# Kernel optimization log

Hardware: AMD Instinct MI355X
Metric: run time of the kernel (lower is better)

Reference implementation:

```python
import jax, jax.numpy as jnp
import numpy as np

DIM = 512
BATCH, SEQ = 4, 4096


def setup_inputs() -> dict:
    key = jax.random.key(0)
    kx, kq, kk, kv, ko = jax.random.split(key, 5)
    s = DIM ** -0.5  # fan-in style init scale for stability
    return {
        "x": jax.random.normal(kx, (BATCH, SEQ, DIM), dtype=jnp.float32),
        "Wq": jax.random.normal(kq, (DIM, DIM), dtype=jnp.float32) * s,
        "Wk": jax.random.normal(kk, (DIM, DIM), dtype=jnp.float32) * s,
        "Wv": jax.random.normal(kv, (DIM, DIM), dtype=jnp.float32) * s,
        "Wo": jax.random.normal(ko, (DIM, DIM), dtype=jnp.float32) * s,
    }


def reference(x, Wq, Wk, Wv, Wo):
    # x: [B, S, D]; projections (torch Linear, no bias -> x @ W here)
    q = jnp.einsum('bsd,dk->bsk', x, Wq)  # [B,S,K]
    k = jnp.einsum('bsd,dk->bsk', x, Wk)  # [B,S,K]
    v = jnp.einsum('bsd,dv->bsv', x, Wv)  # [B,S,V]

    # sequential recurrence: M_t = M_{t-1} + v_t k_t^T ; y_t = M_t q_t
    def step(M, qkv_t):
        q_t, k_t, v_t = qkv_t  # each [B, K] / [B, V]
        M = M + v_t[:, :, None] * k_t[:, None, :]  # [B, V, K]
        y_t = jnp.einsum('bvk,bk->bv', M, q_t)
        return M, y_t

    M0 = jnp.zeros((x.shape[0], Wv.shape[1], Wk.shape[1]), dtype=x.dtype)
    qT = jnp.swapaxes(q, 0, 1)  # [S,B,K]
    kT = jnp.swapaxes(k, 0, 1)
    vT = jnp.swapaxes(v, 0, 1)
    _, ys = jax.lax.scan(step, M0, (qT, kT, vT))  # ys: [S,B,V]
    y = jnp.swapaxes(ys, 0, 1)  # [B,S,V]
    return jnp.einsum('bsv,vd->bsd', y, Wo)
```

## Files before the change

### kernel.cpp

```cpp
#include <hip/hip_runtime.h>
#include <hip/hip_bf16.h>

typedef __attribute__((ext_vector_type(8))) short bf16x8;
typedef __attribute__((ext_vector_type(4))) float f32x4;

__device__ inline short f2bf(float f) {
    __hip_bfloat16 h = __float2bfloat16(f);
    short s;
    __builtin_memcpy(&s, &h, 2);
    return s;
}
__device__ inline float bf2f(short s) {
    unsigned int u = ((unsigned int)(unsigned short)s) << 16;
    float f;
    __builtin_memcpy(&f, &u, 4);
    return f;
}

__device__ inline void cp16_async(const void* g, void* l) {
    __builtin_amdgcn_global_load_lds(
        (const __attribute__((address_space(1))) void*)g,
        (__attribute__((address_space(3))) void*)l, 16, 0, 0);
}


__global__ void prep_kernel(const float* __restrict__ x, short* __restrict__ Xb,
                            const float* __restrict__ W0, const float* __restrict__ W1,
                            const float* __restrict__ W2, const float* __restrict__ W3,
                            short* __restrict__ W4T) {
    int bid = blockIdx.x;
    if (bid < 8192) {
        int i = bid * 256 + threadIdx.x;
        float4 f = ((const float4*)x)[i];
        union { short s[4]; int2 v; } u;
        u.s[0] = f2bf(f.x); u.s[1] = f2bf(f.y); u.s[2] = f2bf(f.z); u.s[3] = f2bf(f.w);
        ((int2*)Xb)[i] = u.v;
    } else {
        int i = (bid - 8192) * 256 + threadIdx.x;
        int w = i >> 18;
        int r = i & 262143;
        int n = r >> 9, k = r & 511;
        const float* W = (w == 0) ? W0 : (w == 1) ? W1 : (w == 2) ? W2 : W3;
        W4T[i] = f2bf(W[k * 512 + n]);
    }
}


#define LDS_DECL __shared__ short sA0[4096], sA1[4096], sB0[4096], sB1[4096]

__device__ inline void mfma_kloop64(const short* __restrict__ A, int lda,
                                    const short* __restrict__ B, int ldb,
                                    int Kd, f32x4* acc,
                                    short* sA0, short* sA1, short* sB0, short* sB1) {
    const int tid = threadIdx.x, lane = tid & 63, wv = tid >> 6;
    const int quad = lane >> 4, lr = lane & 15;
    const int wr = (wv >> 1) * 64, wc = (wv & 1) * 64;
    const int c0 = tid, c1 = tid + 256;
    const int r0 = c0 >> 2, k80 = (c0 & 3) * 8;
    const int r1 = c1 >> 2, k81 = (c1 & 3) * 8;

    for (int k0 = 0; k0 < Kd; k0 += 64) {
        __syncthreads();
        cp16_async(A + (size_t)r0 * lda + k0 + k80,      sA0 + c0 * 8);
        cp16_async(A + (size_t)r1 * lda + k0 + k81,      sA0 + c1 * 8);
        cp16_async(A + (size_t)r0 * lda + k0 + 32 + k80, sA1 + c0 * 8);
        cp16_async(A + (size_t)r1 * lda + k0 + 32 + k81, sA1 + c1 * 8);
        cp16_async(B + (size_t)r0 * ldb + k0 + k80,      sB0 + c0 * 8);
        cp16_async(B + (size_t)r1 * ldb + k0 + k81,      sB0 + c1 * 8);
        cp16_async(B + (size_t)r0 * ldb + k0 + 32 + k80, sB1 + c0 * 8);
        cp16_async(B + (size_t)r1 * ldb + k0 + 32 + k81, sB1 + c1 * 8);
        __syncthreads();
#pragma unroll
        for (int half = 0; half < 2; ++half) {
            const short* pa = half ? sA1 : sA0;
            const short* pb = half ? sB1 : sB0;
            bf16x8 af[4], bfr[4];
#pragma unroll
            for (int i = 0; i < 4; ++i)
                af[i] = *(const bf16x8*)&pa[(wr + i * 16 + lr) * 32 + quad * 8];
#pragma unroll
            for (int j = 0; j < 4; ++j)
                bfr[j] = *(const bf16x8*)&pb[(wc + j * 16 + lr) * 32 + quad * 8];
#pragma unroll
            for (int i = 0; i < 4; ++i)
#pragma unroll
                for (int j = 0; j < 4; ++j)
                    acc[i * 4 + j] = __builtin_amdgcn_mfma_f32_16x16x32_bf16(af[i], bfr[j], acc[i * 4 + j], 0, 0, 0);
        }
    }
}

__device__ inline void store_out(float* p, float v) { *p = v; }
__device__ inline void store_out(short* p, float v) { *p = f2bf(v); }

template <typename OutT>
__device__ inline void store_tile128(OutT* C, int ldc, const f32x4* acc) {
    const int lane = threadIdx.x & 63, wv = threadIdx.x >> 6;
    const int quad = lane >> 4, lr = lane & 15;
    const int wr = (wv >> 1) * 64, wc = (wv & 1) * 64;
#pragma unroll
    for (int i = 0; i < 4; ++i)
#pragma unroll
        for (int j = 0; j < 4; ++j)
#pragma unroll
            for (int r = 0; r < 4; ++r)
                store_out(&C[(size_t)(wr + i * 16 + quad * 4 + r) * ldc + wc + j * 16 + lr],
                          acc[i * 4 + j][r]);
}

__global__ __launch_bounds__(256, 4) void proj_all(const short* __restrict__ Xb,
                                                   const short* __restrict__ W4T,
                                                   short* __restrict__ Qb, short* __restrict__ Kb,
                                                   short* __restrict__ Vt, short* __restrict__ Kt) {
    LDS_DECL;
    f32x4 acc[16];
#pragma unroll
    for (int i = 0; i < 16; ++i) acc[i] = (f32x4){0.f, 0.f, 0.f, 0.f};
    const int bid = blockIdx.x;
    const int lane = threadIdx.x & 63, wv = threadIdx.x >> 6;
    const int quad = lane >> 4, lr = lane & 15;
    const int wr = (wv >> 1) * 64, wc = (wv & 1) * 64;
    if (bid < 1024) {
        const int mt = bid >> 3, by = bid & 7;
        const short* At = Xb + (size_t)mt * 128 * 512;
        const short* Bt = W4T + (size_t)by * 128 * 512;
        short* Ct = ((by < 4) ? Qb : Kb) + (size_t)mt * 128 * 512 + (by & 3) * 128;
        mfma_kloop64(At, 512, Bt, 512, 512, acc, sA0, sA1, sB0, sB1);
        store_tile128(Ct, 512, acc);
        if (by >= 4) {
            const int b = mt >> 5;
            const int t0b = (mt & 31) * 128;
            const int f0 = (by - 4) * 128;
#pragma unroll
            for (int i = 0; i < 4; ++i)
#pragma unroll
                for (int j = 0; j < 4; ++j) {
                    int f = f0 + wc + j * 16 + lr;
                    int tt0 = t0b + wr + i * 16 + quad * 4;
                    short tmp[4];
#pragma unroll
                    for (int r = 0; r < 4; ++r) tmp[r] = f2bf(acc[i * 4 + j][r]);
                    *(int2*)&Kt[((size_t)b * 512 + f) * 4096 + tt0] = *(const int2*)tmp;
                }
        }
    } else {
        const int r = bid - 1024;
        const int b = r & 3, tt = (r >> 2) & 31, ft = r >> 7;
        const short* At = W4T + (size_t)2 * 262144 + (size_t)ft * 128 * 512;
        const short* Bt = Xb + ((size_t)b * 4096 + tt * 128) * 512;
        short* Ct = Vt + (size_t)b * 512 * 4096 + (size_t)ft * 128 * 4096 + tt * 128;
        mfma_kloop64(At, 512, Bt, 512, 512, acc, sA0, sA1, sB0, sB1);
        store_tile128(Ct, 4096, acc);
    }
}


__global__ __launch_bounds__(256, 4) void phaseA(const short* __restrict__ Vt,
                                                 const short* __restrict__ Kt,
                                                 short* __restrict__ AM) {
    LDS_DECL;
    const int bc = blockIdx.z, b = bc >> 4, c = bc & 15;
    const short* Ap = Vt + ((size_t)b * 512 + blockIdx.x * 128) * 4096 + c * 256;
    const short* Bp = Kt + ((size_t)b * 512 + blockIdx.y * 128) * 4096 + c * 256;
    short* Cp = AM + (size_t)bc * 262144 + (size_t)blockIdx.x * 128 * 512 + blockIdx.y * 128;
    f32x4 acc[16];
#pragma unroll
    for (int i = 0; i < 16; ++i) acc[i] = (f32x4){0.f, 0.f, 0.f, 0.f};
    mfma_kloop64(Ap, 4096, Bp, 4096, 256, acc, sA0, sA1, sB0, sB1);
    store_tile128(Cp, 512, acc);
}

__global__ __launch_bounds__(256, 4) void scan_phaseS(short* __restrict__ AM,
                                                      const short* __restrict__ Q,
                                                      const short* __restrict__ K,
                                                      short* __restrict__ P) {
    LDS_DECL;
    if (blockIdx.x < 512) {
        int i = blockIdx.x * 256 + threadIdx.x;
        int b = i >> 15;
        int vk8 = i & 32767;
        size_t base = (size_t)b * 16 * 262144 + (size_t)vk8 * 8;
        float acc[8];
#pragma unroll
        for (int s = 0; s < 8; ++s) acc[s] = 0.f;
        for (int c = 0; c < 16; ++c) {
            short* p = AM + base + (size_t)c * 262144;
            short in8[8];
            *(int4*)in8 = *(const int4*)p;
            short out8[8];
#pragma unroll
            for (int s = 0; s < 8; ++s) out8[s] = f2bf(acc[s]);
            *(int4*)p = *(const int4*)out8;
#pragma unroll
            for (int s = 0; s < 8; ++s) acc[s] += bf2f(in8[s]);
        }
        return;
    }
    const int e = blockIdx.x - 512;
    const int bc = e >> 2, mt = e & 1, nt = (e >> 1) & 1;
    if (mt < nt) return;
    const int b = bc >> 4, c = bc & 15;
    short* Pt = P + (size_t)bc * 65536 + (size_t)mt * 128 * 256 + nt * 128;
    const short* Ap = Q + ((size_t)(b * 4096 + c * 256 + mt * 128)) * 512;
    const short* Bp = K + ((size_t)(b * 4096 + c * 256 + nt * 128)) * 512;
    f32x4 acc[16];
#pragma unroll
    for (int i = 0; i < 16; ++i) acc[i] = (f32x4){0.f, 0.f, 0.f, 0.f};
    mfma_kloop64(Ap, 512, Bp, 512, 512, acc, sA0, sA1, sB0, sB1);
    const int lane = threadIdx.x & 63, wv = threadIdx.x >> 6;
    const int quad = lane >> 4, lr = lane & 15;
    const int wr = (wv >> 1) * 64, wc = (wv & 1) * 64;
    const bool diag = (mt == nt);
#pragma unroll
    for (int i = 0; i < 4; ++i)
#pragma unroll
        for (int j = 0; j < 4; ++j)
#pragma unroll
            for (int r = 0; r < 4; ++r) {
                int t = wr + i * 16 + quad * 4 + r;
                int jj = wc + j * 16 + lr;
                float v = (!diag || jj <= t) ? acc[i * 4 + j][r] : 0.f;
                Pt[(size_t)t * 256 + jj] = f2bf(v);
            }
}

__global__ __launch_bounds__(256, 4) void phaseY(const short* __restrict__ Q,
                                                 const short* __restrict__ Mpre,
                                                 const short* __restrict__ P,
                                                 const short* __restrict__ Vt,
                                                 short* __restrict__ Y) {
    LDS_DECL;
    const int bc = blockIdx.z, b = bc >> 4, c = bc & 15;
    const int mt = blockIdx.x, nt = blockIdx.y;
    f32x4 acc[16];
#pragma unroll
    for (int i = 0; i < 16; ++i) acc[i] = (f32x4){0.f, 0.f, 0.f, 0.f};
    const short* Ai = Q + ((size_t)(b * 4096 + c * 256 + mt * 128)) * 512;
    const short* Bi = Mpre + (size_t)bc * 262144 + (size_t)nt * 128 * 512;
    mfma_kloop64(Ai, 512, Bi, 512, 512, acc, sA0, sA1, sB0, sB1);
    const short* Ap = P + (size_t)bc * 65536 + (size_t)mt * 128 * 256;
    const short* Bv = Vt + ((size_t)b * 512 + nt * 128) * 4096 + c * 256;
    mfma_kloop64(Ap, 256, Bv, 4096, (mt + 1) * 128, acc, sA0, sA1, sB0, sB1);
    short* Cp = Y + ((size_t)(b * 4096 + c * 256 + mt * 128)) * 512 + nt * 128;
    store_tile128(Cp, 512, acc);
}

template <typename OutT>
__global__ __launch_bounds__(256, 4) void gemm128(const short* __restrict__ A, int lda,
                                                  const short* __restrict__ B, int ldb,
                                                  OutT* __restrict__ C, int ldc, int Kd) {
    LDS_DECL;
    const short* At = A + (size_t)blockIdx.x * 128 * lda;
    const short* Bt = B + (size_t)blockIdx.y * 128 * ldb;
    OutT* Ct = C + (size_t)blockIdx.x * 128 * ldc + blockIdx.y * 128;
    f32x4 acc[16];
#pragma unroll
    for (int i = 0; i < 16; ++i) acc[i] = (f32x4){0.f, 0.f, 0.f, 0.f};
    mfma_kloop64(At, lda, Bt, ldb, Kd, acc, sA0, sA1, sB0, sB1);
    store_tile128(Ct, ldc, acc);
}


extern "C" void kernel_launch(void* const* d_in, const int* in_sizes, int n_in,
                              void* d_out, int out_size, void* d_ws, size_t ws_size,
                              hipStream_t stream) {
    const float* x  = (const float*)d_in[0];
    const float* Wq = (const float*)d_in[1];
    const float* Wk = (const float*)d_in[2];
    const float* Wv = (const float*)d_in[3];
    const float* Wo = (const float*)d_in[4];
    float* out = (float*)d_out;

    const size_t NTD = 16384 * 512;

    short* ws  = (short*)d_ws;
    short* Xb  = ws;
    short* Qb  = Xb + NTD;
    short* Kb  = Qb + NTD;
    short* Kt  = Kb + NTD;
    short* Vt  = Kt + NTD;
    short* P   = Vt + NTD;
    short* W4T = P + 4194304;
    short* AM  = W4T + 1048576;
    short* Yb  = Kb;

    short* WoT = W4T + 3 * 262144;

    prep_kernel<<<12288, 256, 0, stream>>>(x, Xb, Wq, Wk, Wv, Wo, W4T);
    proj_all<<<1536, 256, 0, stream>>>(Xb, W4T, Qb, Kb, Vt, Kt);
    phaseA<<<dim3(4, 4, 64), 256, 0, stream>>>(Vt, Kt, AM);
    scan_phaseS<<<768, 256, 0, stream>>>(AM, Qb, Kb, P);
    phaseY<<<dim3(2, 4, 64), 256, 0, stream>>>(Qb, AM, P, Vt, Yb);
    gemm128<float><<<dim3(128, 4), 256, 0, stream>>>(Yb, 512, WoT, 512, out, 512, 512);
}
```

Baseline: 222.0 us.

## Fuse all phases into one cooperative persistent kernel with grid syncs

Replaces the six separate kernel launches with one cooperative kernel that loops over virtual block indices for each phase, separated by grid-wide syncs. This removes per-launch overhead and the gaps between kernels. In exchange the grid is capped at 512 persistent blocks, launch bounds drop to 2 blocks per CU, and grid.sync barriers add their own cost. Phase bodies that do uneven work may also load-balance worse. The multi-kernel path is kept as a fallback if the cooperative launch fails.

```diff
diff --git a/kernel.cpp b/kernel.cpp
--- a/kernel.cpp
+++ b/kernel.cpp
@@ -1,5 +1,8 @@
 #include <hip/hip_runtime.h>
 #include <hip/hip_bf16.h>
+#include <hip/hip_cooperative_groups.h>
+
+namespace cg = cooperative_groups;
 
 typedef __attribute__((ext_vector_type(8))) short bf16x8;
 typedef __attribute__((ext_vector_type(4))) float f32x4;
@@ -23,30 +26,6 @@
         (__attribute__((address_space(3))) void*)l, 16, 0, 0);
 }
 
-
-__global__ void prep_kernel(const float* __restrict__ x, short* __restrict__ Xb,
-                            const float* __restrict__ W0, const float* __restrict__ W1,
-                            const float* __restrict__ W2, const float* __restrict__ W3,
-                            short* __restrict__ W4T) {
-    int bid = blockIdx.x;
-    if (bid < 8192) {
-        int i = bid * 256 + threadIdx.x;
-        float4 f = ((const float4*)x)[i];
-        union { short s[4]; int2 v; } u;
-        u.s[0] = f2bf(f.x); u.s[1] = f2bf(f.y); u.s[2] = f2bf(f.z); u.s[3] = f2bf(f.w);
-        ((int2*)Xb)[i] = u.v;
-    } else {
-        int i = (bid - 8192) * 256 + threadIdx.x;
-        int w = i >> 18;
-        int r = i & 262143;
-        int n = r >> 9, k = r & 511;
-        const float* W = (w == 0) ? W0 : (w == 1) ? W1 : (w == 2) ? W2 : W3;
-        W4T[i] = f2bf(W[k * 512 + n]);
-    }
-}
-
-
-#define LDS_DECL __shared__ short sA0[4096], sA1[4096], sB0[4096], sB1[4096]
 
 __device__ inline void mfma_kloop64(const short* __restrict__ A, int lda,
                                     const short* __restrict__ B, int ldb,
@@ -108,20 +87,38 @@
                           acc[i * 4 + j][r]);
 }
 
-__global__ __launch_bounds__(256, 4) void proj_all(const short* __restrict__ Xb,
-                                                   const short* __restrict__ W4T,
-                                                   short* __restrict__ Qb, short* __restrict__ Kb,
-                                                   short* __restrict__ Vt, short* __restrict__ Kt) {
-    LDS_DECL;
-    f32x4 acc[16];
-#pragma unroll
-    for (int i = 0; i < 16; ++i) acc[i] = (f32x4){0.f, 0.f, 0.f, 0.f};
-    const int bid = blockIdx.x;
+
+__device__ inline void body_prep(int vb, const float* x, short* Xb,
+                                 const float* Wq, const float* Wk,
+                                 const float* Wv, const float* Wo, short* W4T) {
+    const int tid = threadIdx.x;
+    if (vb < 8192) {
+        int i = vb * 256 + tid;
+        float4 f = ((const float4*)x)[i];
+        union { short s[4]; int2 v; } u;
+        u.s[0] = f2bf(f.x); u.s[1] = f2bf(f.y); u.s[2] = f2bf(f.z); u.s[3] = f2bf(f.w);
+        ((int2*)Xb)[i] = u.v;
+    } else {
+        int i = (vb - 8192) * 256 + tid;
+        int w = i >> 18;
+        int r = i & 262143;
+        int n = r >> 9, k = r & 511;
+        const float* W = (w == 0) ? Wq : (w == 1) ? Wk : (w == 2) ? Wv : Wo;
+        W4T[i] = f2bf(W[k * 512 + n]);
+    }
+}
+
+__device__ inline void body_proj(int vb, const short* Xb, const short* W4T,
+                                 short* Qb, short* Kb, short* Vt, short* Kt,
+                                 short* sA0, short* sA1, short* sB0, short* sB1) {
     const int lane = threadIdx.x & 63, wv = threadIdx.x >> 6;
     const int quad = lane >> 4, lr = lane & 15;
     const int wr = (wv >> 1) * 64, wc = (wv & 1) * 64;
-    if (bid < 1024) {
-        const int mt = bid >> 3, by = bid & 7;
+    f32x4 acc[16];
+#pragma unroll
+    for (int i = 0; i < 16; ++i) acc[i] = (f32x4){0.f, 0.f, 0.f, 0.f};
+    if (vb < 1024) {
+        const int mt = vb >> 3, by = vb & 7;
         const short* At = Xb + (size_t)mt * 128 * 512;
         const short* Bt = W4T + (size_t)by * 128 * 512;
         short* Ct = ((by < 4) ? Qb : Kb) + (size_t)mt * 128 * 512 + (by & 3) * 128;
@@ -144,7 +141,7 @@
                 }
         }
     } else {
-        const int r = bid - 1024;
+        const int r = vb - 1024;
         const int b = r & 3, tt = (r >> 2) & 31, ft = r >> 7;
         const short* At = W4T + (size_t)2 * 262144 + (size_t)ft * 128 * 512;
         const short* Bt = Xb + ((size_t)b * 4096 + tt * 128) * 512;
@@ -154,15 +151,13 @@
     }
 }
 
-
-__global__ __launch_bounds__(256, 4) void phaseA(const short* __restrict__ Vt,
-                                                 const short* __restrict__ Kt,
-                                                 short* __restrict__ AM) {
-    LDS_DECL;
-    const int bc = blockIdx.z, b = bc >> 4, c = bc & 15;
-    const short* Ap = Vt + ((size_t)b * 512 + blockIdx.x * 128) * 4096 + c * 256;
-    const short* Bp = Kt + ((size_t)b * 512 + blockIdx.y * 128) * 4096 + c * 256;
-    short* Cp = AM + (size_t)bc * 262144 + (size_t)blockIdx.x * 128 * 512 + blockIdx.y * 128;
+__device__ inline void body_phaseA(int vb, const short* Vt, const short* Kt, short* AM,
+                                   short* sA0, short* sA1, short* sB0, short* sB1) {
+    const int xt = vb & 3, yt = (vb >> 2) & 3, bc = vb >> 4;
+    const int b = bc >> 4, c = bc & 15;
+    const short* Ap = Vt + ((size_t)b * 512 + xt * 128) * 4096 + c * 256;
+    const short* Bp = Kt + ((size_t)b * 512 + yt * 128) * 4096 + c * 256;
+    short* Cp = AM + (size_t)bc * 262144 + (size_t)xt * 128 * 512 + yt * 128;
     f32x4 acc[16];
 #pragma unroll
     for (int i = 0; i < 16; ++i) acc[i] = (f32x4){0.f, 0.f, 0.f, 0.f};
@@ -170,13 +165,12 @@
     store_tile128(Cp, 512, acc);
 }
 
-__global__ __launch_bounds__(256, 4) void scan_phaseS(short* __restrict__ AM,
-                                                      const short* __restrict__ Q,
-                                                      const short* __restrict__ K,
-                                                      short* __restrict__ P) {
-    LDS_DECL;
-    if (blockIdx.x < 512) {
-        int i = blockIdx.x * 256 + threadIdx.x;
+__device__ inline void body_scan_phaseS(int vb, short* AM, const short* Qb, const short* Kb,
+                                        short* P,
+                                        short* sA0, short* sA1, short* sB0, short* sB1) {
+    const int tid = threadIdx.x;
+    if (vb < 512) {
+        int i = vb * 256 + tid;
         int b = i >> 15;
         int vk8 = i & 32767;
         size_t base = (size_t)b * 16 * 262144 + (size_t)vk8 * 8;
@@ -196,18 +190,18 @@
         }
         return;
     }
-    const int e = blockIdx.x - 512;
+    const int e = vb - 512;
     const int bc = e >> 2, mt = e & 1, nt = (e >> 1) & 1;
     if (mt < nt) return;
     const int b = bc >> 4, c = bc & 15;
     short* Pt = P + (size_t)bc * 65536 + (size_t)mt * 128 * 256 + nt * 128;
-    const short* Ap = Q + ((size_t)(b * 4096 + c * 256 + mt * 128)) * 512;
-    const short* Bp = K + ((size_t)(b * 4096 + c * 256 + nt * 128)) * 512;
+    const short* Ap = Qb + ((size_t)(b * 4096 + c * 256 + mt * 128)) * 512;
+    const short* Bp = Kb + ((size_t)(b * 4096 + c * 256 + nt * 128)) * 512;
     f32x4 acc[16];
 #pragma unroll
     for (int i = 0; i < 16; ++i) acc[i] = (f32x4){0.f, 0.f, 0.f, 0.f};
     mfma_kloop64(Ap, 512, Bp, 512, 512, acc, sA0, sA1, sB0, sB1);
-    const int lane = threadIdx.x & 63, wv = threadIdx.x >> 6;
+    const int lane = tid & 63, wv = tid >> 6;
     const int quad = lane >> 4, lr = lane & 15;
     const int wr = (wv >> 1) * 64, wc = (wv & 1) * 64;
     const bool diag = (mt == nt);
@@ -224,40 +218,117 @@
             }
 }
 
-__global__ __launch_bounds__(256, 4) void phaseY(const short* __restrict__ Q,
-                                                 const short* __restrict__ Mpre,
-                                                 const short* __restrict__ P,
-                                                 const short* __restrict__ Vt,
-                                                 short* __restrict__ Y) {
-    LDS_DECL;
-    const int bc = blockIdx.z, b = bc >> 4, c = bc & 15;
-    const int mt = blockIdx.x, nt = blockIdx.y;
-    f32x4 acc[16];
-#pragma unroll
-    for (int i = 0; i < 16; ++i) acc[i] = (f32x4){0.f, 0.f, 0.f, 0.f};
-    const short* Ai = Q + ((size_t)(b * 4096 + c * 256 + mt * 128)) * 512;
+__device__ inline void body_phaseY(int vb, const short* Qb, const short* Mpre,
+                                   const short* P, const short* Vt, short* Yb,
+                                   short* sA0, short* sA1, short* sB0, short* sB1) {
+    const int mt = vb & 1, nt = (vb >> 1) & 3, bc = vb >> 3;
+    const int b = bc >> 4, c = bc & 15;
+    f32x4 acc[16];
+#pragma unroll
+    for (int i = 0; i < 16; ++i) acc[i] = (f32x4){0.f, 0.f, 0.f, 0.f};
+    const short* Ai = Qb + ((size_t)(b * 4096 + c * 256 + mt * 128)) * 512;
     const short* Bi = Mpre + (size_t)bc * 262144 + (size_t)nt * 128 * 512;
     mfma_kloop64(Ai, 512, Bi, 512, 512, acc, sA0, sA1, sB0, sB1);
     const short* Ap = P + (size_t)bc * 65536 + (size_t)mt * 128 * 256;
     const short* Bv = Vt + ((size_t)b * 512 + nt * 128) * 4096 + c * 256;
     mfma_kloop64(Ap, 256, Bv, 4096, (mt + 1) * 128, acc, sA0, sA1, sB0, sB1);
-    short* Cp = Y + ((size_t)(b * 4096 + c * 256 + mt * 128)) * 512 + nt * 128;
+    short* Cp = Yb + ((size_t)(b * 4096 + c * 256 + mt * 128)) * 512 + nt * 128;
     store_tile128(Cp, 512, acc);
 }
 
-template <typename OutT>
-__global__ __launch_bounds__(256, 4) void gemm128(const short* __restrict__ A, int lda,
-                                                  const short* __restrict__ B, int ldb,
-                                                  OutT* __restrict__ C, int ldc, int Kd) {
-    LDS_DECL;
-    const short* At = A + (size_t)blockIdx.x * 128 * lda;
-    const short* Bt = B + (size_t)blockIdx.y * 128 * ldb;
-    OutT* Ct = C + (size_t)blockIdx.x * 128 * ldc + blockIdx.y * 128;
-    f32x4 acc[16];
-#pragma unroll
-    for (int i = 0; i < 16; ++i) acc[i] = (f32x4){0.f, 0.f, 0.f, 0.f};
-    mfma_kloop64(At, lda, Bt, ldb, Kd, acc, sA0, sA1, sB0, sB1);
-    store_tile128(Ct, ldc, acc);
+__device__ inline void body_outproj(int vb, const short* Yb, const short* W4T, float* out,
+                                    short* sA0, short* sA1, short* sB0, short* sB1) {
+    const int mt = vb >> 2, nt = vb & 3;
+    const short* At = Yb + (size_t)mt * 128 * 512;
+    const short* Bt = W4T + (size_t)3 * 262144 + (size_t)nt * 128 * 512;
+    float* Ct = out + (size_t)mt * 128 * 512 + nt * 128;
+    f32x4 acc[16];
+#pragma unroll
+    for (int i = 0; i < 16; ++i) acc[i] = (f32x4){0.f, 0.f, 0.f, 0.f};
+    mfma_kloop64(At, 512, Bt, 512, 512, acc, sA0, sA1, sB0, sB1);
+    store_tile128(Ct, 512, acc);
+}
+
+
+__global__ __launch_bounds__(256, 2) void fused_all(
+    const float* __restrict__ x,
+    const float* __restrict__ Wq, const float* __restrict__ Wk,
+    const float* __restrict__ Wv, const float* __restrict__ Wo,
+    short* __restrict__ Xb, short* __restrict__ W4T,
+    short* __restrict__ Qb, short* __restrict__ Kb,
+    short* __restrict__ Kt, short* __restrict__ Vt,
+    short* __restrict__ P, short* __restrict__ AM,
+    float* __restrict__ out)
+{
+    __shared__ short sA0[4096], sA1[4096], sB0[4096], sB1[4096];
+    cg::grid_group grid = cg::this_grid();
+    const int nb = gridDim.x;
+    short* Yb = Kb;
+
+    for (int vb = blockIdx.x; vb < 12288; vb += nb)
+        body_prep(vb, x, Xb, Wq, Wk, Wv, Wo, W4T);
+    grid.sync();
+    for (int vb = blockIdx.x; vb < 1536; vb += nb)
+        body_proj(vb, Xb, W4T, Qb, Kb, Vt, Kt, sA0, sA1, sB0, sB1);
+    grid.sync();
+    for (int vb = blockIdx.x; vb < 1024; vb += nb)
+        body_phaseA(vb, Vt, Kt, AM, sA0, sA1, sB0, sB1);
+    grid.sync();
+    for (int vb = blockIdx.x; vb < 768; vb += nb)
+        body_scan_phaseS(vb, AM, Qb, Kb, P, sA0, sA1, sB0, sB1);
+    grid.sync();
+    for (int vb = blockIdx.x; vb < 512; vb += nb)
+        body_phaseY(vb, Qb, AM, P, Vt, Yb, sA0, sA1, sB0, sB1);
+    grid.sync();
+    for (int vb = blockIdx.x; vb < 512; vb += nb)
+        body_outproj(vb, Yb, W4T, out, sA0, sA1, sB0, sB1);
+}
+
+
+__global__ void prep_kernel(const float* __restrict__ x, short* __restrict__ Xb,
+                            const float* __restrict__ W0, const float* __restrict__ W1,
+                            const float* __restrict__ W2, const float* __restrict__ W3,
+                            short* __restrict__ W4T) {
+    body_prep(blockIdx.x, x, Xb, W0, W1, W2, W3, W4T);
+}
+
+__global__ __launch_bounds__(256, 2) void proj_all(const short* __restrict__ Xb,
+                                                   const short* __restrict__ W4T,
+                                                   short* __restrict__ Qb, short* __restrict__ Kb,
+                                                   short* __restrict__ Vt, short* __restrict__ Kt) {
+    __shared__ short sA0[4096], sA1[4096], sB0[4096], sB1[4096];
+    body_proj(blockIdx.x, Xb, W4T, Qb, Kb, Vt, Kt, sA0, sA1, sB0, sB1);
+}
+
+__global__ __launch_bounds__(256, 2) void phaseA_k(const short* __restrict__ Vt,
+                                                   const short* __restrict__ Kt,
+                                                   short* __restrict__ AM) {
+    __shared__ short sA0[4096], sA1[4096], sB0[4096], sB1[4096];
+    body_phaseA(blockIdx.x, Vt, Kt, AM, sA0, sA1, sB0, sB1);
+}
+
+__global__ __launch_bounds__(256, 2) void scan_phaseS_k(short* __restrict__ AM,
+                                                        const short* __restrict__ Q,
+                                                        const short* __restrict__ K,
+                                                        short* __restrict__ P) {
+    __shared__ short sA0[4096], sA1[4096], sB0[4096], sB1[4096];
+    body_scan_phaseS(blockIdx.x, AM, Q, K, P, sA0, sA1, sB0, sB1);
+}
+
+__global__ __launch_bounds__(256, 2) void phaseY_k(const short* __restrict__ Q,
+                                                   const short* __restrict__ Mpre,
+                                                   const short* __restrict__ P,
+                                                   const short* __restrict__ Vt,
+                                                   short* __restrict__ Y) {
+    __shared__ short sA0[4096], sA1[4096], sB0[4096], sB1[4096];
+    body_phaseY(blockIdx.x, Q, Mpre, P, Vt, Y, sA0, sA1, sB0, sB1);
+}
+
+__global__ __launch_bounds__(256, 2) void outproj_k(const short* __restrict__ Y,
+                                                    const short* __restrict__ W4T,
+                                                    float* __restrict__ out) {
+    __shared__ short sA0[4096], sA1[4096], sB0[4096], sB1[4096];
+    body_outproj(blockIdx.x, Y, W4T, out, sA0, sA1, sB0, sB1);
 }
 
 
@@ -284,12 +355,27 @@
     short* AM  = W4T + 1048576;
     short* Yb  = Kb;
 
-    short* WoT = W4T + 3 * 262144;
+    int maxb = 0;
+    hipError_t qerr = hipOccupancyMaxActiveBlocksPerMultiprocessor(
+        &maxb, (const void*)fused_all, 256, 0);
+    hipError_t lerr = hipErrorUnknown;
+    if (qerr == hipSuccess && maxb > 0) {
+        int nblk = maxb * 256;
+        if (nblk > 512) nblk = 512;
+        void* args[] = {
+            (void*)&x, (void*)&Wq, (void*)&Wk, (void*)&Wv, (void*)&Wo,
+            (void*)&Xb, (void*)&W4T, (void*)&Qb, (void*)&Kb, (void*)&Kt,
+            (void*)&Vt, (void*)&P, (void*)&AM, (void*)&out
+        };
+        lerr = hipLaunchCooperativeKernel((const void*)fused_all, dim3(nblk),
+                                          dim3(256), args, 0, stream);
+    }
+    if (lerr == hipSuccess) return;
 
     prep_kernel<<<12288, 256, 0, stream>>>(x, Xb, Wq, Wk, Wv, Wo, W4T);
     proj_all<<<1536, 256, 0, stream>>>(Xb, W4T, Qb, Kb, Vt, Kt);
-    phaseA<<<dim3(4, 4, 64), 256, 0, stream>>>(Vt, Kt, AM);
-    scan_phaseS<<<768, 256, 0, stream>>>(AM, Qb, Kb, P);
-    phaseY<<<dim3(2, 4, 64), 256, 0, stream>>>(Qb, AM, P, Vt, Yb);
-    gemm128<float><<<dim3(128, 4), 256, 0, stream>>>(Yb, 512, WoT, 512, out, 512, 512);
-}
+    phaseA_k<<<1024, 256, 0, stream>>>(Vt, Kt, AM);
+    scan_phaseS_k<<<768, 256, 0, stream>>>(AM, Qb, Kb, P);
+    phaseY_k<<<512, 256, 0, stream>>>(Qb, AM, P, Vt, Yb);
+    outproj_k<<<512, 256, 0, stream>>>(Yb, W4T, out);
+}
```

Result: slower. 435.8 us (+96.3%).

## Double-buffer GEMM k-loop with async prefetch and tile weight transpose via LDS

Applied to the files above, without the earlier changes.

Replaces the single-stage 64-wide k-loop, which synchronised twice per step, with a double-buffered 32-wide loop. It prefetches the next k-slice into the alternate LDS buffer while MFMAs run on the current one. The weight transpose in prep now goes through a shared-memory tile, so global reads and writes are coalesced instead of strided per element. Launch bounds drop to 2 waves per SIMD and grids are flattened to 1D. This may lower occupancy and halves the MFMA work per barrier.

```diff
diff --git a/kernel.cpp b/kernel.cpp
--- a/kernel.cpp
+++ b/kernel.cpp
@@ -23,35 +23,51 @@
         (__attribute__((address_space(3))) void*)l, 16, 0, 0);
 }
 
-
 __global__ void prep_kernel(const float* __restrict__ x, short* __restrict__ Xb,
                             const float* __restrict__ W0, const float* __restrict__ W1,
                             const float* __restrict__ W2, const float* __restrict__ W3,
                             short* __restrict__ W4T) {
-    int bid = blockIdx.x;
+    __shared__ short sT[64][72];
+    const int bid = blockIdx.x, tid = threadIdx.x;
     if (bid < 8192) {
-        int i = bid * 256 + threadIdx.x;
+        int i = bid * 256 + tid;
         float4 f = ((const float4*)x)[i];
         union { short s[4]; int2 v; } u;
         u.s[0] = f2bf(f.x); u.s[1] = f2bf(f.y); u.s[2] = f2bf(f.z); u.s[3] = f2bf(f.w);
         ((int2*)Xb)[i] = u.v;
-    } else {
-        int i = (bid - 8192) * 256 + threadIdx.x;
-        int w = i >> 18;
-        int r = i & 262143;
-        int n = r >> 9, k = r & 511;
-        const float* W = (w == 0) ? W0 : (w == 1) ? W1 : (w == 2) ? W2 : W3;
-        W4T[i] = f2bf(W[k * 512 + n]);
-    }
-}
-
-
-#define LDS_DECL __shared__ short sA0[4096], sA1[4096], sB0[4096], sB1[4096]
-
-__device__ inline void mfma_kloop64(const short* __restrict__ A, int lda,
-                                    const short* __restrict__ B, int ldb,
-                                    int Kd, f32x4* acc,
-                                    short* sA0, short* sA1, short* sB0, short* sB1) {
+        return;
+    }
+    const int wb = bid - 8192;
+    const int w = wb >> 6, r = wb & 63;
+    const int n0 = (r >> 3) * 64, k0 = (r & 7) * 64;
+    const float* W = (w == 0) ? W0 : (w == 1) ? W1 : (w == 2) ? W2 : W3;
+#pragma unroll
+    for (int rr = 0; rr < 4; ++rr) {
+        int c = rr * 256 + tid;
+        int row = c >> 4, col4 = (c & 15) * 4;
+        float4 f = *(const float4*)&W[(size_t)(k0 + row) * 512 + n0 + col4];
+        sT[col4 + 0][row] = f2bf(f.x);
+        sT[col4 + 1][row] = f2bf(f.y);
+        sT[col4 + 2][row] = f2bf(f.z);
+        sT[col4 + 3][row] = f2bf(f.w);
+    }
+    __syncthreads();
+#pragma unroll
+    for (int rr = 0; rr < 2; ++rr) {
+        int c = rr * 256 + tid;
+        int f = c >> 3, k8 = (c & 7) * 8;
+        int4 v = *(const int4*)&sT[f][k8];
+        *(int4*)&W4T[(size_t)w * 262144 + (size_t)(n0 + f) * 512 + k0 + k8] = v;
+    }
+}
+
+
+#define LDS_DBUF __shared__ short sA[8192], sB[8192]
+
+__device__ inline void mfma_kloop_dbuf(const short* __restrict__ A, int lda,
+                                       const short* __restrict__ B, int ldb,
+                                       int Kd, f32x4* acc,
+                                       short* sA, short* sB) {
     const int tid = threadIdx.x, lane = tid & 63, wv = tid >> 6;
     const int quad = lane >> 4, lr = lane & 15;
     const int wr = (wv >> 1) * 64, wc = (wv & 1) * 64;
@@ -59,34 +75,39 @@
     const int r0 = c0 >> 2, k80 = (c0 & 3) * 8;
     const int r1 = c1 >> 2, k81 = (c1 & 3) * 8;
 
-    for (int k0 = 0; k0 < Kd; k0 += 64) {
+    __syncthreads();
+    cp16_async(A + (size_t)r0 * lda + k80, sA + c0 * 8);
+    cp16_async(A + (size_t)r1 * lda + k81, sA + c1 * 8);
+    cp16_async(B + (size_t)r0 * ldb + k80, sB + c0 * 8);
+    cp16_async(B + (size_t)r1 * ldb + k81, sB + c1 * 8);
+
+    int cur = 0;
+    for (int k0 = 0; k0 < Kd; k0 += 32) {
         __syncthreads();
-        cp16_async(A + (size_t)r0 * lda + k0 + k80,      sA0 + c0 * 8);
-        cp16_async(A + (size_t)r1 * lda + k0 + k81,      sA0 + c1 * 8);
-        cp16_async(A + (size_t)r0 * lda + k0 + 32 + k80, sA1 + c0 * 8);
-        cp16_async(A + (size_t)r1 * lda + k0 + 32 + k81, sA1 + c1 * 8);
-        cp16_async(B + (size_t)r0 * ldb + k0 + k80,      sB0 + c0 * 8);
-        cp16_async(B + (size_t)r1 * ldb + k0 + k81,      sB0 + c1 * 8);
-        cp16_async(B + (size_t)r0 * ldb + k0 + 32 + k80, sB1 + c0 * 8);
-        cp16_async(B + (size_t)r1 * ldb + k0 + 32 + k81, sB1 + c1 * 8);
-        __syncthreads();
-#pragma unroll
-        for (int half = 0; half < 2; ++half) {
-            const short* pa = half ? sA1 : sA0;
-            const short* pb = half ? sB1 : sB0;
-            bf16x8 af[4], bfr[4];
-#pragma unroll
-            for (int i = 0; i < 4; ++i)
-                af[i] = *(const bf16x8*)&pa[(wr + i * 16 + lr) * 32 + quad * 8];
+        const int nxt = cur ^ 1;
+        if (k0 + 32 < Kd) {
+            const short* An = A + k0 + 32;
+            const short* Bn = B + k0 + 32;
+            cp16_async(An + (size_t)r0 * lda + k80, sA + nxt * 4096 + c0 * 8);
+            cp16_async(An + (size_t)r1 * lda + k81, sA + nxt * 4096 + c1 * 8);
+            cp16_async(Bn + (size_t)r0 * ldb + k80, sB + nxt * 4096 + c0 * 8);
+            cp16_async(Bn + (size_t)r1 * ldb + k81, sB + nxt * 4096 + c1 * 8);
+        }
+        const short* pa = sA + cur * 4096;
+        const short* pb = sB + cur * 4096;
+        bf16x8 af[4], bfr[4];
+#pragma unroll
+        for (int i = 0; i < 4; ++i)
+            af[i] = *(const bf16x8*)&pa[(wr + i * 16 + lr) * 32 + quad * 8];
+#pragma unroll
+        for (int j = 0; j < 4; ++j)
+            bfr[j] = *(const bf16x8*)&pb[(wc + j * 16 + lr) * 32 + quad * 8];
+#pragma unroll
+        for (int i = 0; i < 4; ++i)
 #pragma unroll
             for (int j = 0; j < 4; ++j)
-                bfr[j] = *(const bf16x8*)&pb[(wc + j * 16 + lr) * 32 + quad * 8];
-#pragma unroll
-            for (int i = 0; i < 4; ++i)
-#pragma unroll
-                for (int j = 0; j < 4; ++j)
-                    acc[i * 4 + j] = __builtin_amdgcn_mfma_f32_16x16x32_bf16(af[i], bfr[j], acc[i * 4 + j], 0, 0, 0);
-        }
+                acc[i * 4 + j] = __builtin_amdgcn_mfma_f32_16x16x32_bf16(af[i], bfr[j], acc[i * 4 + j], 0, 0, 0);
+        cur = nxt;
     }
 }
 
@@ -108,11 +129,11 @@
                           acc[i * 4 + j][r]);
 }
 
-__global__ __launch_bounds__(256, 4) void proj_all(const short* __restrict__ Xb,
+__global__ __launch_bounds__(256, 2) void proj_all(const short* __restrict__ Xb,
                                                    const short* __restrict__ W4T,
                                                    short* __restrict__ Qb, short* __restrict__ Kb,
                                                    short* __restrict__ Vt, short* __restrict__ Kt) {
-    LDS_DECL;
+    LDS_DBUF;
     f32x4 acc[16];
 #pragma unroll
     for (int i = 0; i < 16; ++i) acc[i] = (f32x4){0.f, 0.f, 0.f, 0.f};
@@ -125,7 +146,7 @@
         const short* At = Xb + (size_t)mt * 128 * 512;
         const short* Bt = W4T + (size_t)by * 128 * 512;
         short* Ct = ((by < 4) ? Qb : Kb) + (size_t)mt * 128 * 512 + (by & 3) * 128;
-        mfma_kloop64(At, 512, Bt, 512, 512, acc, sA0, sA1, sB0, sB1);
+        mfma_kloop_dbuf(At, 512, Bt, 512, 512, acc, sA, sB);
         store_tile128(Ct, 512, acc);
         if (by >= 4) {
             const int b = mt >> 5;
@@ -149,34 +170,36 @@
         const short* At = W4T + (size_t)2 * 262144 + (size_t)ft * 128 * 512;
         const short* Bt = Xb + ((size_t)b * 4096 + tt * 128) * 512;
         short* Ct = Vt + (size_t)b * 512 * 4096 + (size_t)ft * 128 * 4096 + tt * 128;
-        mfma_kloop64(At, 512, Bt, 512, 512, acc, sA0, sA1, sB0, sB1);
+        mfma_kloop_dbuf(At, 512, Bt, 512, 512, acc, sA, sB);
         store_tile128(Ct, 4096, acc);
     }
 }
 
-
-__global__ __launch_bounds__(256, 4) void phaseA(const short* __restrict__ Vt,
-                                                 const short* __restrict__ Kt,
-                                                 short* __restrict__ AM) {
-    LDS_DECL;
-    const int bc = blockIdx.z, b = bc >> 4, c = bc & 15;
-    const short* Ap = Vt + ((size_t)b * 512 + blockIdx.x * 128) * 4096 + c * 256;
-    const short* Bp = Kt + ((size_t)b * 512 + blockIdx.y * 128) * 4096 + c * 256;
-    short* Cp = AM + (size_t)bc * 262144 + (size_t)blockIdx.x * 128 * 512 + blockIdx.y * 128;
-    f32x4 acc[16];
-#pragma unroll
-    for (int i = 0; i < 16; ++i) acc[i] = (f32x4){0.f, 0.f, 0.f, 0.f};
-    mfma_kloop64(Ap, 4096, Bp, 4096, 256, acc, sA0, sA1, sB0, sB1);
+__global__ __launch_bounds__(256, 2) void phaseA_k(const short* __restrict__ Vt,
+                                                   const short* __restrict__ Kt,
+                                                   short* __restrict__ AM) {
+    LDS_DBUF;
+    const int vb = blockIdx.x;
+    const int xt = vb & 3, yt = (vb >> 2) & 3, bc = vb >> 4;
+    const int b = bc >> 4, c = bc & 15;
+    const short* Ap = Vt + ((size_t)b * 512 + xt * 128) * 4096 + c * 256;
+    const short* Bp = Kt + ((size_t)b * 512 + yt * 128) * 4096 + c * 256;
+    short* Cp = AM + (size_t)bc * 262144 + (size_t)xt * 128 * 512 + yt * 128;
+    f32x4 acc[16];
+#pragma unroll
+    for (int i = 0; i < 16; ++i) acc[i] = (f32x4){0.f, 0.f, 0.f, 0.f};
+    mfma_kloop_dbuf(Ap, 4096, Bp, 4096, 256, acc, sA, sB);
     store_tile128(Cp, 512, acc);
 }
 
-__global__ __launch_bounds__(256, 4) void scan_phaseS(short* __restrict__ AM,
-                                                      const short* __restrict__ Q,
-                                                      const short* __restrict__ K,
-                                                      short* __restrict__ P) {
-    LDS_DECL;
+__global__ __launch_bounds__(256, 2) void scan_phaseS_k(short* __restrict__ AM,
+                                                        const short* __restrict__ Q,
+                                                        const short* __restrict__ K,
+                                                        short* __restrict__ P) {
+    LDS_DBUF;
+    const int tid = threadIdx.x;
     if (blockIdx.x < 512) {
-        int i = blockIdx.x * 256 + threadIdx.x;
+        int i = blockIdx.x * 256 + tid;
         int b = i >> 15;
         int vk8 = i & 32767;
         size_t base = (size_t)b * 16 * 262144 + (size_t)vk8 * 8;
@@ -206,8 +229,8 @@
     f32x4 acc[16];
 #pragma unroll
     for (int i = 0; i < 16; ++i) acc[i] = (f32x4){0.f, 0.f, 0.f, 0.f};
-    mfma_kloop64(Ap, 512, Bp, 512, 512, acc, sA0, sA1, sB0, sB1);
-    const int lane = threadIdx.x & 63, wv = threadIdx.x >> 6;
+    mfma_kloop_dbuf(Ap, 512, Bp, 512, 512, acc, sA, sB);
+    const int lane = tid & 63, wv = tid >> 6;
     const int quad = lane >> 4, lr = lane & 15;
     const int wr = (wv >> 1) * 64, wc = (wv & 1) * 64;
     const bool diag = (mt == nt);
@@ -224,40 +247,41 @@
             }
 }
 
-__global__ __launch_bounds__(256, 4) void phaseY(const short* __restrict__ Q,
-                                                 const short* __restrict__ Mpre,
-                                                 const short* __restrict__ P,
-                                                 const short* __restrict__ Vt,
-                                                 short* __restrict__ Y) {
-    LDS_DECL;
-    const int bc = blockIdx.z, b = bc >> 4, c = bc & 15;
-    const int mt = blockIdx.x, nt = blockIdx.y;
+__global__ __launch_bounds__(256, 2) void phaseY_k(const short* __restrict__ Q,
+                                                   const short* __restrict__ Mpre,
+                                                   const short* __restrict__ P,
+                                                   const short* __restrict__ Vt,
+                                                   short* __restrict__ Y) {
+    LDS_DBUF;
+    const int vb = blockIdx.x;
+    const int mt = vb & 1, nt = (vb >> 1) & 3, bc = vb >> 3;
+    const int b = bc >> 4, c = bc & 15;
     f32x4 acc[16];
 #pragma unroll
     for (int i = 0; i < 16; ++i) acc[i] = (f32x4){0.f, 0.f, 0.f, 0.f};
     const short* Ai = Q + ((size_t)(b * 4096 + c * 256 + mt * 128)) * 512;
     const short* Bi = Mpre + (size_t)bc * 262144 + (size_t)nt * 128 * 512;
-    mfma_kloop64(Ai, 512, Bi, 512, 512, acc, sA0, sA1, sB0, sB1);
+    mfma_kloop_dbuf(Ai, 512, Bi, 512, 512, acc, sA, sB);
     const short* Ap = P + (size_t)bc * 65536 + (size_t)mt * 128 * 256;
     const short* Bv = Vt + ((size_t)b * 512 + nt * 128) * 4096 + c * 256;
-    mfma_kloop64(Ap, 256, Bv, 4096, (mt + 1) * 128, acc, sA0, sA1, sB0, sB1);
+    mfma_kloop_dbuf(Ap, 256, Bv, 4096, (mt + 1) * 128, acc, sA, sB);
     short* Cp = Y + ((size_t)(b * 4096 + c * 256 + mt * 128)) * 512 + nt * 128;
     store_tile128(Cp, 512, acc);
 }
 
-template <typename OutT>
-__global__ __launch_bounds__(256, 4) void gemm128(const short* __restrict__ A, int lda,
-                                                  const short* __restrict__ B, int ldb,
-                                                  OutT* __restrict__ C, int ldc, int Kd) {
-    LDS_DECL;
-    const short* At = A + (size_t)blockIdx.x * 128 * lda;
-    const short* Bt = B + (size_t)blockIdx.y * 128 * ldb;
-    OutT* Ct = C + (size_t)blockIdx.x * 128 * ldc + blockIdx.y * 128;
-    f32x4 acc[16];
-#pragma unroll
-    for (int i = 0; i < 16; ++i) acc[i] = (f32x4){0.f, 0.f, 0.f, 0.f};
-    mfma_kloop64(At, lda, Bt, ldb, Kd, acc, sA0, sA1, sB0, sB1);
-    store_tile128(Ct, ldc, acc);
+__global__ __launch_bounds__(256, 2) void outproj_k(const short* __restrict__ Y,
+                                                    const short* __restrict__ W4T,
+                                                    float* __restrict__ out) {
+    LDS_DBUF;
+    const int mt = blockIdx.x >> 2, nt = blockIdx.x & 3;
+    const short* At = Y + (size_t)mt * 128 * 512;
+    const short* Bt = W4T + (size_t)3 * 262144 + (size_t)nt * 128 * 512;
+    float* Ct = out + (size_t)mt * 128 * 512 + nt * 128;
+    f32x4 acc[16];
+#pragma unroll
+    for (int i = 0; i < 16; ++i) acc[i] = (f32x4){0.f, 0.f, 0.f, 0.f};
+    mfma_kloop_dbuf(At, 512, Bt, 512, 512, acc, sA, sB);
+    store_tile128(Ct, 512, acc);
 }
 
 
@@ -284,12 +308,10 @@
     short* AM  = W4T + 1048576;
     short* Yb  = Kb;
 
-    short* WoT = W4T + 3 * 262144;
-
-    prep_kernel<<<12288, 256, 0, stream>>>(x, Xb, Wq, Wk, Wv, Wo, W4T);
+    prep_kernel<<<8448, 256, 0, stream>>>(x, Xb, Wq, Wk, Wv, Wo, W4T);
     proj_all<<<1536, 256, 0, stream>>>(Xb, W4T, Qb, Kb, Vt, Kt);
-    phaseA<<<dim3(4, 4, 64), 256, 0, stream>>>(Vt, Kt, AM);
-    scan_phaseS<<<768, 256, 0, stream>>>(AM, Qb, Kb, P);
-    phaseY<<<dim3(2, 4, 64), 256, 0, stream>>>(Qb, AM, P, Vt, Yb);
-    gemm128<float><<<dim3(128, 4), 256, 0, stream>>>(Yb, 512, WoT, 512, out, 512, 512);
-}
+    phaseA_k<<<1024, 256, 0, stream>>>(Vt, Kt, AM);
+    scan_phaseS_k<<<768, 256, 0, stream>>>(AM, Qb, Kb, P);
+    phaseY_k<<<512, 256, 0, stream>>>(Qb, AM, P, Vt, Yb);
+    outproj_k<<<512, 256, 0, stream>>>(Yb, W4T, out);
+}
```

After: 233.9 us. +5.3%, slower.
